# Performance work log

Hardware: AMD Instinct MI355X
Metric: run time of the kernel (lower is better)

Reference implementation:

```python
import jax, jax.numpy as jnp
import numpy as np

B, NQ, NK = 4, 2048, 2048
DQ = DK = DV = 512
H = 8
DS = DV // H  # 64


def _layernorm(x, g, b, eps=1e-5):
    m = jnp.mean(x, axis=-1, keepdims=True)
    v = jnp.var(x, axis=-1, keepdims=True)
    return (x - m) * jax.lax.rsqrt(v + eps) * g + b


def setup_inputs() -> dict:
    key = jax.random.key(0)
    ks = jax.random.split(key, 16)
    def lin(k, fan_in, fan_out):
        # torch nn.Linear default init: U(-1/sqrt(fan_in), 1/sqrt(fan_in))
        bound = 1.0 / np.sqrt(fan_in)
        k1, k2 = jax.random.split(k)
        W = jax.random.uniform(k1, (fan_in, fan_out), jnp.float32, -bound, bound)
        b = jax.random.uniform(k2, (fan_out,), jnp.float32, -bound, bound)
        return W, b
    Wq, bq = lin(ks[0], DQ, DV)
    Wk, bk = lin(ks[1], DK, DV)
    Wv, bv = lin(ks[2], DK, DV)
    W0, b0 = lin(ks[3], DV, DV)
    W1, b1 = lin(ks[4], DV, DV)
    # xavier_uniform for kp/vp of shape (1, DS): bound = sqrt(6/(1+DS))
    xb = np.sqrt(6.0 / (1 + DS))
    kp = jax.random.uniform(ks[5], (DS,), jnp.float32, -xb, xb)
    vp = jax.random.uniform(ks[6], (DS,), jnp.float32, -xb, xb)
    return {
        "Q": jax.random.normal(ks[7], (B, NQ, DQ), jnp.float32),
        "K": jax.random.normal(ks[8], (B, NK, DK), jnp.float32),
        "Kpos": jax.random.uniform(ks[9], (B, NQ, NK), jnp.float32),
        "Wq": Wq, "bq": bq, "Wk": Wk, "bk": bk, "Wv": Wv, "bv": bv,
        "kp": kp, "vp": vp,
        "W0": W0, "b0": b0, "W1": W1, "b1": b1,
        "g0": jnp.ones((DV,), jnp.float32), "be0": jnp.zeros((DV,), jnp.float32),
        "g1": jnp.ones((DV,), jnp.float32), "be1": jnp.zeros((DV,), jnp.float32),
    }


def reference(Q, K, Kpos, Wq, bq, Wk, bk, Wv, bv, kp, vp, W0, b0, W1, b1, g0, be0, g1, be1):
    Qp = Q @ Wq + bq                       # [B,NQ,DV]
    Kp = K @ Wk + bk                       # [B,NK,DV]
    Vp = K @ Wv + bv                       # [B,NK,DV]
    # head split (torch split/cat along batch == reshape to [B,N,H,DS])
    Qh = Qp.reshape(B, NQ, H, DS)
    Kh = Kp.reshape(B, NK, H, DS)
    Vh = Vp.reshape(B, NK, H, DS)
    scale = 1.0 / np.sqrt(DV)              # NOTE: original scales by sqrt(dim_V), not per-head dim
    scores = jnp.einsum('bqhd,bkhd->bhqk', Qh, Kh) * scale
    # ShawRE key bias: KE[b,h,q,k] = Kpos[b,q,k] * <Qh[b,q,h,:], kp>
    qkp = jnp.einsum('bqhd,d->bhq', Qh, kp)          # [B,H,NQ]
    scores = scores + Kpos[:, None, :, :] * qkp[:, :, :, None]
    A = jax.nn.softmax(scores, axis=-1)              # [B,H,NQ,NK]
    out = jnp.einsum('bhqk,bkhd->bqhd', A, Vh)       # [B,NQ,H,DS]
    # ShawRE value bias: VE[b,q,h,:] = (sum_k A*Kpos) * vp
    akp = jnp.einsum('bhqk,bqk->bhq', A, Kpos)       # [B,H,NQ]
    out = out + akp.transpose(0, 2, 1)[..., None] * vp
    O = (Qh + out).reshape(B, NQ, DV)
    O = _layernorm(O, g0, be0)
    resO = O
    O = jax.nn.relu(O @ W0 + b0)           # fc_o[0] with relu (numlayers=2)
    O = resO + jax.nn.relu(O @ W1 + b1)    # fc_o[-1] + residual
    O = _layernorm(O, g1, be1)
    return O
```

## Files before the change

kernel.cpp:

```cpp
#include <hip/hip_runtime.h>
#include <math.h>

#define Bx  4
#define NQx 2048
#define NKx 2048
#define Dx  512
#define Hx  8

typedef __attribute__((ext_vector_type(8))) __bf16 bf16x8;
typedef __attribute__((ext_vector_type(4))) float f32x4;
typedef __attribute__((ext_vector_type(16))) float f32x16;

typedef const __attribute__((address_space(1))) unsigned int* gas_ptr;
typedef __attribute__((address_space(3))) unsigned int* lds_ptr;

__device__ __forceinline__ void gload16(const void* g, void* l){
  __builtin_amdgcn_global_load_lds((gas_ptr)g, (lds_ptr)l, 16, 0, 0);
}

__device__ __forceinline__ unsigned short f2bf(float f){
  union { float f; unsigned int u; } v; v.f = f;
  unsigned int r = (v.u + 0x7FFFu + ((v.u >> 16) & 1u)) >> 16;
  return (unsigned short)r;
}
__device__ __forceinline__ float bf2f(unsigned short u){
  union { unsigned int u; float f; } v; v.u = ((unsigned int)u) << 16; return v.f;
}
__device__ __forceinline__ unsigned int cvtpk_bf16(float a, float b){
  unsigned int d;
  asm("v_cvt_pk_bf16_f32 %0, %1, %2" : "=v"(d) : "v"(a), "v"(b));
  return d;
}
__device__ __forceinline__ void plane32_swap(unsigned int& a, unsigned int& b){
  asm("v_permlane32_swap_b32 %0, %1" : "+v"(a), "+v"(b));
}
__device__ __forceinline__ float fexp2(float x){
  float d; asm("v_exp_f32 %0, %1" : "=v"(d) : "v"(x)); return d;
}
__device__ __forceinline__ float fmax3(float a, float b, float c){
  float d; asm("v_max3_f32 %0, %1, %2, %3" : "=v"(d) : "v"(a), "v"(b), "v"(c)); return d;
}

__global__ __launch_bounds__(256) void mab_wt(
    const float* __restrict__ Wq, const float* __restrict__ Wk, const float* __restrict__ Wv,
    const float* __restrict__ W0, const float* __restrict__ W1,
    unsigned short* __restrict__ Wt)
{
  __shared__ unsigned short T[64][72];
  const int z = blockIdx.z;
  const float* W = (z==0)?Wq:(z==1)?Wk:(z==2)?Wv:(z==3)?W0:W1;
  unsigned short* O = Wt + (size_t)z*512*512;
  const int k0 = blockIdx.x*64, n0 = blockIdx.y*64;
  const int tid = threadIdx.x;
  #pragma unroll
  for (int i=0;i<4;++i){
    int id = tid + i*256;
    int r = id>>4, c4 = id&15;
    float4 v = *(const float4*)(W + (size_t)(k0+r)*512 + n0 + c4*4);
    ushort4 o; o.x=f2bf(v.x); o.y=f2bf(v.y); o.z=f2bf(v.z); o.w=f2bf(v.w);
    *(ushort4*)&T[r][c4*4] = o;
  }
  __syncthreads();
  #pragma unroll
  for (int i=0;i<2;++i){
    int id = tid + i*256;
    int c = id>>3, r8 = id&7;
    union { unsigned short u[8]; uint4 v; } o;
    #pragma unroll
    for (int j=0;j<8;++j) o.u[j] = T[r8*8+j][c];
    *(uint4*)(O + (size_t)(n0+c)*512 + k0 + r8*8) = o.v;
  }
}

__global__ __launch_bounds__(256) void mab_vt(
    const unsigned short* __restrict__ Vp, unsigned short* __restrict__ Vpt)
{
  __shared__ unsigned short T[64][72];
  const int r0 = blockIdx.x*64;
  const int c0 = blockIdx.y*64;
  const int b  = blockIdx.z;
  const int tid = threadIdx.x;
  #pragma unroll
  for (int i=0;i<2;++i){
    int id = tid + i*256;
    int r = id>>3, c8 = id&7;
    *(uint4*)&T[r][c8*8] = *(const uint4*)(Vp + (size_t)(b*NKx + r0+r)*512 + c0 + c8*8);
  }
  __syncthreads();
  #pragma unroll
  for (int i=0;i<2;++i){
    int id = tid + i*256;
    int c = id>>3, r8 = id&7;
    union { unsigned short u[8]; uint4 v; } o;
    #pragma unroll
    for (int j=0;j<8;++j) o.u[j] = T[r8*8+j][c];
    *(uint4*)(Vpt + ((size_t)(b*512) + c0 + c)*NKx + r0 + r8*8) = o.v;
  }
}

__global__ __launch_bounds__(256) void mab_gemm_proj(
    const float* __restrict__ Qf, const float* __restrict__ Kf,
    const unsigned short* __restrict__ Wt,
    const float* __restrict__ bq, const float* __restrict__ bk, const float* __restrict__ bv,
    unsigned short* __restrict__ Cb, float kscale)
{
  __shared__ unsigned short As[128][64];
  __shared__ unsigned short Bs[128][64];
  const int z = blockIdx.z;
  const float* A = (z==0) ? Qf : Kf;
  const unsigned short* W = Wt + (size_t)z*512*512;
  const float* bias = (z==0)?bq:((z==1)?bk:bv);
  const float sc = (z==1) ? kscale : 1.0f;
  const int m0 = blockIdx.y*128, n0 = blockIdx.x*128;
  const int tid = threadIdx.x, w = tid>>6, lane = tid&63, g = lane>>4, q16 = lane&15;
  const int wr = w>>1, wc = w&1;

  f32x4 acc[4][4];
  #pragma unroll
  for (int m=0;m<4;++m)
    #pragma unroll
    for (int n=0;n<4;++n) acc[m][n] = (f32x4){0.f,0.f,0.f,0.f};

  float4 areg[8];
  #pragma unroll
  for (int i=0;i<8;++i){
    int id = i*256 + tid, row = id>>4, qc = id&15;
    areg[i] = *(const float4*)(A + (size_t)(m0+row)*512 + qc*4);
  }

  for (int k0 = 0; k0 < 512; k0 += 64){
    __syncthreads();
    #pragma unroll
    for (int i=0;i<8;++i){
      int id = i*256 + tid, row = id>>4, qc = id&15;
      unsigned int lo = cvtpk_bf16(areg[i].x, areg[i].y);
      unsigned int hi = cvtpk_bf16(areg[i].z, areg[i].w);
      unsigned int* dst = (unsigned int*)((char*)&As[0][0] + row*128
                          + ((qc>>1) ^ (row&7))*16 + (qc&1)*8);
      dst[0] = lo; dst[1] = hi;
    }
    #pragma unroll
    for (int i=0;i<4;++i){
      int o   = (w*4 + i)*1024 + lane*16;
      int row = o >> 7;
      int c   = (o >> 4) & 7;
      int cs  = c ^ (row & 7);
      gload16(W + (size_t)(n0+row)*512 + k0 + cs*8, (char*)&Bs[0][0] + (w*4+i)*1024);
    }
    __syncthreads();
    if (k0 + 64 < 512){
      #pragma unroll
      for (int i=0;i<8;++i){
        int id = i*256 + tid, row = id>>4, qc = id&15;
        areg[i] = *(const float4*)(A + (size_t)(m0+row)*512 + (k0+64) + qc*4);
      }
    }
    #pragma unroll
    for (int ks=0;ks<2;++ks){
      bf16x8 af[4], bfr[4];
      #pragma unroll
      for (int m=0;m<4;++m){
        int row = wr*64 + m*16 + q16;
        int c   = (ks*4 + g) ^ (row & 7);
        af[m] = *(const bf16x8*)((const char*)&As[0][0] + row*128 + c*16);
      }
      #pragma unroll
      for (int n=0;n<4;++n){
        int row = wc*64 + n*16 + q16;
        int c   = (ks*4 + g) ^ (row & 7);
        bfr[n] = *(const bf16x8*)((const char*)&Bs[0][0] + row*128 + c*16);
      }
      #pragma unroll
      for (int m=0;m<4;++m)
        #pragma unroll
        for (int n=0;n<4;++n)
          acc[m][n] = __builtin_amdgcn_mfma_f32_16x16x32_bf16(af[m], bfr[n], acc[m][n], 0,0,0);
    }
  }

  const size_t ZS = (size_t)8192*512;
  #pragma unroll
  for (int m=0;m<4;++m){
    const int rowl = wr*64 + m*16 + g*4;
    #pragma unroll
    for (int n=0;n<4;++n){
      const int col = n0 + wc*64 + n*16 + q16;
      const float bv2 = bias[col];
      #pragma unroll
      for (int r=0;r<4;++r){
        float v = (acc[m][n][r] + bv2) * sc;
        Cb[(size_t)z*ZS + (size_t)(m0 + rowl + r)*512 + col] = f2bf(v);
      }
    }
  }
}

__global__ __launch_bounds__(256) void mab_gemm_mlp(
    const unsigned short* __restrict__ A, const unsigned short* __restrict__ W,
    const float* __restrict__ bias, const unsigned short* __restrict__ resb,
    unsigned short* __restrict__ Cb, int relu)
{
  __shared__ unsigned short As[64][64];
  __shared__ unsigned short Bs[64][64];
  const int m0 = blockIdx.y*64, n0 = blockIdx.x*64;
  const int tid = threadIdx.x, w = tid>>6, lane = tid&63, g = lane>>4, q16 = lane&15;
  const int wr = w>>1, wc = w&1;

  f32x4 acc[2][2];
  #pragma unroll
  for (int m=0;m<2;++m)
    #pragma unroll
    for (int n=0;n<2;++n) acc[m][n] = (f32x4){0.f,0.f,0.f,0.f};

  for (int k0 = 0; k0 < 512; k0 += 64){
    __syncthreads();
    #pragma unroll
    for (int i=0;i<2;++i){
      int o   = w*2048 + i*1024 + lane*16;
      int row = o >> 7;
      int c   = (o >> 4) & 7;
      int cs  = c ^ (row & 7);
      gload16(A + (size_t)(m0+row)*512 + k0 + cs*8, (char*)&As[0][0] + w*2048 + i*1024);
      gload16(W + (size_t)(n0+row)*512 + k0 + cs*8, (char*)&Bs[0][0] + w*2048 + i*1024);
    }
    __syncthreads();
    #pragma unroll
    for (int ks=0;ks<2;++ks){
      bf16x8 af[2], bfr[2];
      #pragma unroll
      for (int m=0;m<2;++m){
        int row = wr*32 + m*16 + q16;
        int c   = (ks*4 + g) ^ (row & 7);
        af[m] = *(const bf16x8*)((const char*)&As[0][0] + row*128 + c*16);
      }
      #pragma unroll
      for (int n=0;n<2;++n){
        int row = wc*32 + n*16 + q16;
        int c   = (ks*4 + g) ^ (row & 7);
        bfr[n] = *(const bf16x8*)((const char*)&Bs[0][0] + row*128 + c*16);
      }
      #pragma unroll
      for (int m=0;m<2;++m)
        #pragma unroll
        for (int n=0;n<2;++n)
          acc[m][n] = __builtin_amdgcn_mfma_f32_16x16x32_bf16(af[m], bfr[n], acc[m][n], 0,0,0);
    }
  }

  #pragma unroll
  for (int m=0;m<2;++m){
    const int rowl = wr*32 + m*16 + g*4;
    #pragma unroll
    for (int n=0;n<2;++n){
      const int col = n0 + wc*32 + n*16 + q16;
      const float bv = bias[col];
      #pragma unroll
      for (int r=0;r<4;++r){
        float v = acc[m][n][r] + bv;
        if (relu) v = fmaxf(v, 0.f);
        size_t off = (size_t)(m0 + rowl + r)*512 + col;
        if (resb) v += bf2f(resb[off]);
        Cb[off] = f2bf(v);
      }
    }
  }
}

__global__ __launch_bounds__(512, 2) void mab_attn8(
    const unsigned short* __restrict__ Qp, const unsigned short* __restrict__ Kp,
    const unsigned short* __restrict__ Vpt,
    const float* __restrict__ Kpos, const float* __restrict__ kp, const float* __restrict__ vp,
    const float* __restrict__ g0, const float* __restrict__ be0,
    unsigned short* __restrict__ O0b)
{
  __shared__ __align__(16) char pool[139264];
  const int qt = blockIdx.x;
  const int b  = blockIdx.y;
  const int q0 = qt*32;
  const int tid = threadIdx.x, w = tid>>6, lane = tid&63;
  const int q32 = lane & 31, hi = lane >> 5;
  const int h = w;

  char* Kbase = pool + w*8192;
  char* Vbase = pool + 65536 + w*8192;
  char* KQb   = pool + 131072;

  const unsigned short* Kg = Kp + ((size_t)b*NKx)*Dx + h*64;
  const unsigned short* Vg = Vpt + ((size_t)(b*512) + h*64)*NKx;
  const float* KPg = Kpos + (size_t)b*NQx*NKx + (size_t)q0*NKx;

  const int sr8 = lane>>3, sc8 = lane&7;
  const int sr4 = lane>>2, sc4 = lane&3;

  auto STAGE = [&](int t){
    if (t >= 64) return;
    const int buf = t & 1;
    const int k1 = t*32;
    #pragma unroll
    for (int i=0;i<4;++i){
      int kr = i*8 + sr8, kcs = sc8 ^ (kr & 7);
      gload16(Kg + (size_t)(k1 + kr)*Dx + kcs*8, Kbase + buf*4096 + i*1024);
      int vr = i*16 + sr4, vcs = sc4 ^ ((vr>>1) & 3);
      gload16(Vg + (size_t)vr*NKx + k1 + vcs*8, Vbase + buf*4096 + i*1024);
    }
    if (w < 4){
      int pr = w*8 + sr8, pcs = sc8 ^ (pr & 7);
      gload16(KPg + (size_t)pr*NKx + k1 + pcs*4, KQb + buf*4096 + w*1024);
    }
  };

  auto LOADREGS = [&](int buf, f32x4 (&kq)[4], bf16x8 (&vf)[2][2]){
    #pragma unroll
    for (int a=0;a<4;++a){
      int cc = (a*2 + hi) ^ (q32 & 7);
      kq[a] = *(const f32x4*)(KQb + buf*4096 + q32*128 + cc*16);
    }
    #pragma unroll
    for (int c2=0;c2<2;++c2)
      #pragma unroll
      for (int db=0;db<2;++db){
        int row = db*32 + q32;
        int cc  = (c2*2 + hi) ^ ((row>>1) & 3);
        vf[c2][db] = *(const bf16x8*)(Vbase + buf*4096 + row*64 + cc*16);
      }
  };

  const unsigned short* Qrowp = Qp + ((size_t)(b*NQx + q0 + q32))*Dx + h*64;
  bf16x8 qf[4];
  #pragma unroll
  for (int ds=0; ds<4; ++ds)
    qf[ds] = *(const bf16x8*)(Qrowp + ds*16 + hi*8);

  auto QKT = [&](int buf, f32x16& sT){
    #pragma unroll
    for (int r=0;r<16;++r) sT[r] = 0.f;
    #pragma unroll
    for (int ds=0; ds<4; ++ds){
      int cc = (ds*2 + hi) ^ (q32 & 7);
      bf16x8 kf = *(const bf16x8*)(Kbase + buf*4096 + q32*128 + cc*16);
      sT = __builtin_amdgcn_mfma_f32_32x32x16_bf16(kf, qf[ds], sT, 0,0,0);
    }
  };

  float qkp = 0.f;
  #pragma unroll
  for (int ds=0; ds<4; ++ds){
    union { bf16x8 v; unsigned short u[8]; } qa; qa.v = qf[ds];
    #pragma unroll
    for (int j=0;j<8;++j)
      qkp = fmaf(bf2f(qa.u[j]), kp[ds*16 + hi*8 + j], qkp);
  }
  qkp += __shfl_xor(qkp, 32);
  qkp *= 1.4426950408889634f;

  float m_i = -1e30f, l_i = 0.f, a_i = 0.f;
  f32x16 accT[2];
  #pragma unroll
  for (int db=0; db<2; ++db)
    #pragma unroll
    for (int r=0;r<16;++r) accT[db][r] = 0.f;

  auto FINISH = [&](f32x16& sT, f32x4 (&kq)[4], bf16x8 (&vf)[2][2]){
    #pragma unroll
    for (int r=0;r<16;++r)
      sT[r] = fmaf(kq[r>>2][r&3], qkp, sT[r]);
    float t0 = fmax3(sT[0],  sT[1],  sT[2]);
    float t1 = fmax3(sT[3],  sT[4],  sT[5]);
    float t2 = fmax3(sT[6],  sT[7],  sT[8]);
    float t3 = fmax3(sT[9],  sT[10], sT[11]);
    float t4 = fmax3(sT[12], sT[13], sT[14]);
    float rm = fmax3(fmax3(t0, t1, t2), fmax3(t3, t4, sT[15]), m_i);
    rm = fmaxf(rm, __shfl_xor(rm, 32));
    if (!__all(rm <= m_i + 11.544f)){
      float al = fexp2(m_i - rm);
      m_i = rm;
      l_i *= al; a_i *= al;
      #pragma unroll
      for (int db=0; db<2; ++db)
        #pragma unroll
        for (int r=0;r<16;++r) accT[db][r] *= al;
    }
    float psq[4] = {0.f,0.f,0.f,0.f};
    float pkq[4] = {0.f,0.f,0.f,0.f};
    #pragma unroll
    for (int r=0;r<16;++r){
      float p = fexp2(sT[r] - m_i);
      sT[r] = p;
      psq[r&3] += p;
      pkq[r&3] = fmaf(p, kq[r>>2][r&3], pkq[r&3]);
    }
    float ps = (psq[0]+psq[1]) + (psq[2]+psq[3]);
    float pk = (pkq[0]+pkq[1]) + (pkq[2]+pkq[3]);
    ps += __shfl_xor(ps, 32);
    pk += __shfl_xor(pk, 32);
    l_i += ps; a_i += pk;
    union PW { unsigned int u[4]; bf16x8 v; } pa[2];
    {
      unsigned int w0 = cvtpk_bf16(sT[0],  sT[1]);
      unsigned int w1 = cvtpk_bf16(sT[2],  sT[3]);
      unsigned int w2 = cvtpk_bf16(sT[4],  sT[5]);
      unsigned int w3 = cvtpk_bf16(sT[6],  sT[7]);
      unsigned int w4 = cvtpk_bf16(sT[8],  sT[9]);
      unsigned int w5 = cvtpk_bf16(sT[10], sT[11]);
      unsigned int w6 = cvtpk_bf16(sT[12], sT[13]);
      unsigned int w7 = cvtpk_bf16(sT[14], sT[15]);
      plane32_swap(w0, w2);
      plane32_swap(w1, w3);
      plane32_swap(w4, w6);
      plane32_swap(w5, w7);
      pa[0].u[0]=w0; pa[0].u[1]=w1; pa[0].u[2]=w2; pa[0].u[3]=w3;
      pa[1].u[0]=w4; pa[1].u[1]=w5; pa[1].u[2]=w6; pa[1].u[3]=w7;
    }
    __builtin_amdgcn_s_setprio(1);
    #pragma unroll
    for (int c2=0; c2<2; ++c2){
      #pragma unroll
      for (int db=0; db<2; ++db)
        accT[db] = __builtin_amdgcn_mfma_f32_32x32x16_bf16(vf[c2][db], pa[c2].v, accT[db], 0,0,0);
    }
    __builtin_amdgcn_s_setprio(0);
  };

  STAGE(0);
  __syncthreads();

  f32x16 sT0, sT1;
  f32x4 kq0[4], kq1[4];
  bf16x8 vf0[2][2], vf1[2][2];

  STAGE(1);
  __builtin_amdgcn_sched_barrier(0);
  LOADREGS(0, kq0, vf0);
  QKT(0, sT0);
  __syncthreads();

  for (int t = 1; t < 64; t += 2){
    STAGE(t+1);
    __builtin_amdgcn_sched_barrier(0);
    LOADREGS(1, kq1, vf1);
    QKT(1, sT1);
    FINISH(sT0, kq0, vf0);
    __syncthreads();
    if (t+1 < 64){
      STAGE(t+2);
      __builtin_amdgcn_sched_barrier(0);
      LOADREGS(0, kq0, vf0);
      QKT(0, sT0);
    }
    FINISH(sT1, kq1, vf1);
    __syncthreads();
  }

  float inv = 1.0f / l_i;
  float aw  = a_i * inv;
  float s = 0.f, sq = 0.f;
  #pragma unroll
  for (int db=0; db<2; ++db){
    #pragma unroll
    for (int a2=0; a2<4; ++a2){
      int d0 = db*32 + a2*8 + hi*4;
      f32x4 vpv = *(const f32x4*)(vp + d0);
      ushort4 qh = *(const ushort4*)(Qrowp + d0);
      float o0 = fmaf(accT[db][a2*4+0], inv, bf2f(qh.x) + aw*vpv[0]);
      float o1 = fmaf(accT[db][a2*4+1], inv, bf2f(qh.y) + aw*vpv[1]);
      float o2 = fmaf(accT[db][a2*4+2], inv, bf2f(qh.z) + aw*vpv[2]);
      float o3 = fmaf(accT[db][a2*4+3], inv, bf2f(qh.w) + aw*vpv[3]);
      accT[db][a2*4+0]=o0; accT[db][a2*4+1]=o1;
      accT[db][a2*4+2]=o2; accT[db][a2*4+3]=o3;
      s += (o0+o1)+(o2+o3);
      sq = fmaf(o0,o0, fmaf(o1,o1, fmaf(o2,o2, fmaf(o3,o3, sq))));
    }
  }
  s  += __shfl_xor(s, 32);
  sq += __shfl_xor(sq, 32);
  float* lnred = (float*)pool;
  if (hi == 0){
    lnred[(q32*8 + w)*2 + 0] = s;
    lnred[(q32*8 + w)*2 + 1] = sq;
  }
  __syncthreads();
  float S = 0.f, SQ = 0.f;
  #pragma unroll
  for (int h2=0; h2<8; ++h2){
    S  += lnred[(q32*8 + h2)*2 + 0];
    SQ += lnred[(q32*8 + h2)*2 + 1];
  }
  float mean = S*(1.0f/512.0f);
  float var  = SQ*(1.0f/512.0f) - mean*mean;
  float rstd = rsqrtf(var + 1e-5f);
  unsigned short* Orow = O0b + ((size_t)(b*NQx + q0 + q32))*Dx + h*64;
  #pragma unroll
  for (int db=0; db<2; ++db){
    #pragma unroll
    for (int a2=0; a2<4; ++a2){
      int d0 = db*32 + a2*8 + hi*4;
      f32x4 gg = *(const f32x4*)(g0  + h*64 + d0);
      f32x4 bb = *(const f32x4*)(be0 + h*64 + d0);
      float y0 = (accT[db][a2*4+0]-mean)*rstd*gg[0] + bb[0];
      float y1 = (accT[db][a2*4+1]-mean)*rstd*gg[1] + bb[1];
      float y2 = (accT[db][a2*4+2]-mean)*rstd*gg[2] + bb[2];
      float y3 = (accT[db][a2*4+3]-mean)*rstd*gg[3] + bb[3];
      uint2 pk2;
      pk2.x = cvtpk_bf16(y0, y1);
      pk2.y = cvtpk_bf16(y2, y3);
      *(uint2*)(Orow + d0) = pk2;
    }
  }
}

__global__ __launch_bounds__(256) void mab_ln2b(
    const unsigned short* __restrict__ Xin, const float* __restrict__ g,
    const float* __restrict__ be, float* __restrict__ Yf)
{
  const int row = blockIdx.x;
  const int tid = threadIdx.x;
  ushort2 v2 = *(const ushort2*)(Xin + (size_t)row*Dx + tid*2);
  float vx = bf2f(v2.x), vy = bf2f(v2.y);
  float s  = vx + vy;
  float sq = fmaf(vx,vx, vy*vy);
  #pragma unroll
  for (int m=1; m<64; m<<=1){ s += __shfl_xor(s,m); sq += __shfl_xor(sq,m); }
  __shared__ float red[2][4];
  const int wid = tid>>6, lane = tid&63;
  if (lane==0){ red[0][wid]=s; red[1][wid]=sq; }
  __syncthreads();
  s  = red[0][0]+red[0][1]+red[0][2]+red[0][3];
  sq = red[1][0]+red[1][1]+red[1][2]+red[1][3];
  float mean = s*(1.0f/Dx);
  float var  = sq*(1.0f/Dx) - mean*mean;
  float rstd = rsqrtf(var + 1e-5f);
  float2 gg = *(const float2*)(g  + tid*2);
  float2 bb = *(const float2*)(be + tid*2);
  float2 o;
  o.x = (vx-mean)*rstd*gg.x + bb.x;
  o.y = (vy-mean)*rstd*gg.y + bb.y;
  *(float2*)(Yf + (size_t)row*Dx + tid*2) = o;
}

extern "C" void kernel_launch(void* const* d_in, const int* in_sizes, int n_in,
                              void* d_out, int out_size, void* d_ws, size_t ws_size,
                              hipStream_t stream)
{
  const float* Q    = (const float*)d_in[0];
  const float* K    = (const float*)d_in[1];
  const float* Kpos = (const float*)d_in[2];
  const float* Wq   = (const float*)d_in[3];
  const float* bq   = (const float*)d_in[4];
  const float* Wk   = (const float*)d_in[5];
  const float* bk   = (const float*)d_in[6];
  const float* Wv   = (const float*)d_in[7];
  const float* bv   = (const float*)d_in[8];
  const float* kp   = (const float*)d_in[9];
  const float* vp   = (const float*)d_in[10];
  const float* W0   = (const float*)d_in[11];
  const float* b0   = (const float*)d_in[12];
  const float* W1   = (const float*)d_in[13];
  const float* b1   = (const float*)d_in[14];
  const float* g0   = (const float*)d_in[15];
  const float* be0  = (const float*)d_in[16];
  const float* g1   = (const float*)d_in[17];
  const float* be1  = (const float*)d_in[18];
  float* out = (float*)d_out;
  char* wsb  = (char*)d_ws;

  const size_t MB = 1024*1024;
  unsigned short* Qp  = (unsigned short*)(wsb);
  unsigned short* Kp  = (unsigned short*)(wsb + 8*MB);
  unsigned short* Vp  = (unsigned short*)(wsb + 16*MB);
  unsigned short* Vpt = (unsigned short*)(wsb + 24*MB);
  unsigned short* O0b = (unsigned short*)(wsb + 32*MB);
  unsigned short* Wt  = (unsigned short*)(wsb + 40*MB);
  unsigned short* T2b = (unsigned short*)(wsb + 48*MB);
  unsigned short* T1  = Vp;

  const float kscale = 0.044194173824159216f * 1.4426950408889634f;

  mab_wt<<<dim3(8,8,5), 256, 0, stream>>>(Wq, Wk, Wv, W0, W1, Wt);
  mab_gemm_proj<<<dim3(4,64,3), 256, 0, stream>>>(Q, K, Wt, bq, bk, bv, Qp, kscale);
  mab_vt<<<dim3(32,8,4), 256, 0, stream>>>(Vp, Vpt);
  mab_attn8<<<dim3(64,4), 512, 0, stream>>>(Qp, Kp, Vpt, Kpos, kp, vp, g0, be0, O0b);
  mab_gemm_mlp<<<dim3(8,128), 256, 0, stream>>>(
      O0b, Wt + (size_t)3*512*512, b0, nullptr, T1, 1);
  mab_gemm_mlp<<<dim3(8,128), 256, 0, stream>>>(
      T1, Wt + (size_t)4*512*512, b1, O0b, T2b, 1);
  mab_ln2b<<<8192, 256, 0, stream>>>(T2b, g1, be1, out);
}
```

Before: 183.9 us.

## Split attention over key halves, fuse V transpose into projection, add merge+LN kernel

The attention kernel is split along the key dimension into two halves (flash-decoding style). Each half writes unnormalised partial outputs and its running max/sum statistics, and a new merge kernel combines them and applies the value bias, residual and first layernorm. The grid doubles from 256 to 512 blocks and LDS per block halves, so up to four blocks can be resident per CU. The double-buffered software pipeline is replaced by a single-buffer loop with two barriers per step. The V transpose kernel is removed; the projection GEMM now writes V already transposed. The cost is extra partial-output traffic, one more launch, and less overlap of loads with compute inside the attention loop.

New measurement: 179.0 us. 2.6% less time.

```diff
diff --git a/kernel.cpp b/kernel.cpp
--- a/kernel.cpp
+++ b/kernel.cpp
@@ -72,37 +72,11 @@
   }
 }
 
-__global__ __launch_bounds__(256) void mab_vt(
-    const unsigned short* __restrict__ Vp, unsigned short* __restrict__ Vpt)
-{
-  __shared__ unsigned short T[64][72];
-  const int r0 = blockIdx.x*64;
-  const int c0 = blockIdx.y*64;
-  const int b  = blockIdx.z;
-  const int tid = threadIdx.x;
-  #pragma unroll
-  for (int i=0;i<2;++i){
-    int id = tid + i*256;
-    int r = id>>3, c8 = id&7;
-    *(uint4*)&T[r][c8*8] = *(const uint4*)(Vp + (size_t)(b*NKx + r0+r)*512 + c0 + c8*8);
-  }
-  __syncthreads();
-  #pragma unroll
-  for (int i=0;i<2;++i){
-    int id = tid + i*256;
-    int c = id>>3, r8 = id&7;
-    union { unsigned short u[8]; uint4 v; } o;
-    #pragma unroll
-    for (int j=0;j<8;++j) o.u[j] = T[r8*8+j][c];
-    *(uint4*)(Vpt + ((size_t)(b*512) + c0 + c)*NKx + r0 + r8*8) = o.v;
-  }
-}
-
 __global__ __launch_bounds__(256) void mab_gemm_proj(
     const float* __restrict__ Qf, const float* __restrict__ Kf,
     const unsigned short* __restrict__ Wt,
     const float* __restrict__ bq, const float* __restrict__ bk, const float* __restrict__ bv,
-    unsigned short* __restrict__ Cb, float kscale)
+    unsigned short* __restrict__ Cb, unsigned short* __restrict__ Vpt, float kscale)
 {
   __shared__ unsigned short As[128][64];
   __shared__ unsigned short Bs[128][64];
@@ -186,10 +160,20 @@
     for (int n=0;n<4;++n){
       const int col = n0 + wc*64 + n*16 + q16;
       const float bv2 = bias[col];
-      #pragma unroll
-      for (int r=0;r<4;++r){
-        float v = (acc[m][n][r] + bv2) * sc;
-        Cb[(size_t)z*ZS + (size_t)(m0 + rowl + r)*512 + col] = f2bf(v);
+      float vv[4];
+      #pragma unroll
+      for (int r=0;r<4;++r) vv[r] = (acc[m][n][r] + bv2) * sc;
+      if (z == 2){
+        int rowg0 = m0 + rowl;
+        int bb2 = rowg0 >> 11, kk = rowg0 & 2047;
+        uint2 p2;
+        p2.x = cvtpk_bf16(vv[0], vv[1]);
+        p2.y = cvtpk_bf16(vv[2], vv[3]);
+        *(uint2*)(Vpt + ((size_t)(bb2*512) + col)*2048 + kk) = p2;
+      } else {
+        #pragma unroll
+        for (int r=0;r<4;++r)
+          Cb[(size_t)z*ZS + (size_t)(m0 + rowl + r)*512 + col] = f2bf(vv[r]);
       }
     }
   }
@@ -266,24 +250,26 @@
   }
 }
 
-__global__ __launch_bounds__(512, 2) void mab_attn8(
+__global__ __launch_bounds__(512, 4) void mab_attn9(
     const unsigned short* __restrict__ Qp, const unsigned short* __restrict__ Kp,
     const unsigned short* __restrict__ Vpt,
-    const float* __restrict__ Kpos, const float* __restrict__ kp, const float* __restrict__ vp,
-    const float* __restrict__ g0, const float* __restrict__ be0,
-    unsigned short* __restrict__ O0b)
-{
-  __shared__ __align__(16) char pool[139264];
+    const float* __restrict__ Kpos, const float* __restrict__ kp,
+    unsigned short* __restrict__ OP, float4* __restrict__ MLA)
+{
+  __shared__ __align__(16) char pool[69632];
+
   const int qt = blockIdx.x;
-  const int b  = blockIdx.y;
+  const int ks = blockIdx.y;
+  const int b  = blockIdx.z;
   const int q0 = qt*32;
+  const int kbase = ks*1024;
   const int tid = threadIdx.x, w = tid>>6, lane = tid&63;
   const int q32 = lane & 31, hi = lane >> 5;
   const int h = w;
 
-  char* Kbase = pool + w*8192;
-  char* Vbase = pool + 65536 + w*8192;
-  char* KQb   = pool + 131072;
+  char* Kbase = pool + w*4096;
+  char* Vbase = pool + 32768 + w*4096;
+  char* KQb   = pool + 65536;
 
   const unsigned short* Kg = Kp + ((size_t)b*NKx)*Dx + h*64;
   const unsigned short* Vg = Vpt + ((size_t)(b*512) + h*64)*NKx;
@@ -293,77 +279,71 @@
   const int sr4 = lane>>2, sc4 = lane&3;
 
   auto STAGE = [&](int t){
-    if (t >= 64) return;
-    const int buf = t & 1;
-    const int k1 = t*32;
+    const int k1 = kbase + t*32;
     #pragma unroll
     for (int i=0;i<4;++i){
       int kr = i*8 + sr8, kcs = sc8 ^ (kr & 7);
-      gload16(Kg + (size_t)(k1 + kr)*Dx + kcs*8, Kbase + buf*4096 + i*1024);
+      gload16(Kg + (size_t)(k1 + kr)*Dx + kcs*8, Kbase + i*1024);
       int vr = i*16 + sr4, vcs = sc4 ^ ((vr>>1) & 3);
-      gload16(Vg + (size_t)vr*NKx + k1 + vcs*8, Vbase + buf*4096 + i*1024);
+      gload16(Vg + (size_t)vr*NKx + k1 + vcs*8, Vbase + i*1024);
     }
     if (w < 4){
       int pr = w*8 + sr8, pcs = sc8 ^ (pr & 7);
-      gload16(KPg + (size_t)pr*NKx + k1 + pcs*4, KQb + buf*4096 + w*1024);
+      gload16(KPg + (size_t)pr*NKx + k1 + pcs*4, KQb + w*1024);
     }
   };
 
-  auto LOADREGS = [&](int buf, f32x4 (&kq)[4], bf16x8 (&vf)[2][2]){
+  const unsigned short* Qrowp = Qp + ((size_t)(b*NQx + q0 + q32))*Dx + h*64;
+  bf16x8 qf[4];
+  #pragma unroll
+  for (int ds=0; ds<4; ++ds)
+    qf[ds] = *(const bf16x8*)(Qrowp + ds*16 + hi*8);
+
+  float qkp = 0.f;
+  #pragma unroll
+  for (int ds=0; ds<4; ++ds){
+    union { bf16x8 v; unsigned short u[8]; } qa; qa.v = qf[ds];
+    #pragma unroll
+    for (int j=0;j<8;++j)
+      qkp = fmaf(bf2f(qa.u[j]), kp[ds*16 + hi*8 + j], qkp);
+  }
+  qkp += __shfl_xor(qkp, 32);
+  qkp *= 1.4426950408889634f;
+
+  float m_i = -1e30f, l_i = 0.f, a_i = 0.f;
+  f32x16 accT[2];
+  #pragma unroll
+  for (int db=0; db<2; ++db)
+    #pragma unroll
+    for (int r=0;r<16;++r) accT[db][r] = 0.f;
+
+  STAGE(0);
+  __syncthreads();
+
+  for (int t = 0; t < 32; ++t){
+    f32x16 sT;
+    #pragma unroll
+    for (int r=0;r<16;++r) sT[r] = 0.f;
+    __builtin_amdgcn_s_setprio(1);
+    #pragma unroll
+    for (int ds=0; ds<4; ++ds){
+      int cc = (ds*2 + hi) ^ (q32 & 7);
+      bf16x8 kf = *(const bf16x8*)(Kbase + q32*128 + cc*16);
+      sT = __builtin_amdgcn_mfma_f32_32x32x16_bf16(kf, qf[ds], sT, 0,0,0);
+    }
+    __builtin_amdgcn_s_setprio(0);
+
+    f32x4 kq[4];
     #pragma unroll
     for (int a=0;a<4;++a){
       int cc = (a*2 + hi) ^ (q32 & 7);
-      kq[a] = *(const f32x4*)(KQb + buf*4096 + q32*128 + cc*16);
-    }
-    #pragma unroll
-    for (int c2=0;c2<2;++c2)
-      #pragma unroll
-      for (int db=0;db<2;++db){
-        int row = db*32 + q32;
-        int cc  = (c2*2 + hi) ^ ((row>>1) & 3);
-        vf[c2][db] = *(const bf16x8*)(Vbase + buf*4096 + row*64 + cc*16);
-      }
-  };
-
-  const unsigned short* Qrowp = Qp + ((size_t)(b*NQx + q0 + q32))*Dx + h*64;
-  bf16x8 qf[4];
-  #pragma unroll
-  for (int ds=0; ds<4; ++ds)
-    qf[ds] = *(const bf16x8*)(Qrowp + ds*16 + hi*8);
-
-  auto QKT = [&](int buf, f32x16& sT){
-    #pragma unroll
-    for (int r=0;r<16;++r) sT[r] = 0.f;
-    #pragma unroll
-    for (int ds=0; ds<4; ++ds){
-      int cc = (ds*2 + hi) ^ (q32 & 7);
-      bf16x8 kf = *(const bf16x8*)(Kbase + buf*4096 + q32*128 + cc*16);
-      sT = __builtin_amdgcn_mfma_f32_32x32x16_bf16(kf, qf[ds], sT, 0,0,0);
-    }
-  };
-
-  float qkp = 0.f;
-  #pragma unroll
-  for (int ds=0; ds<4; ++ds){
-    union { bf16x8 v; unsigned short u[8]; } qa; qa.v = qf[ds];
-    #pragma unroll
-    for (int j=0;j<8;++j)
-      qkp = fmaf(bf2f(qa.u[j]), kp[ds*16 + hi*8 + j], qkp);
-  }
-  qkp += __shfl_xor(qkp, 32);
-  qkp *= 1.4426950408889634f;
-
-  float m_i = -1e30f, l_i = 0.f, a_i = 0.f;
-  f32x16 accT[2];
-  #pragma unroll
-  for (int db=0; db<2; ++db)
-    #pragma unroll
-    for (int r=0;r<16;++r) accT[db][r] = 0.f;
-
-  auto FINISH = [&](f32x16& sT, f32x4 (&kq)[4], bf16x8 (&vf)[2][2]){
+      kq[a] = *(const f32x4*)(KQb + q32*128 + cc*16);
+    }
+
     #pragma unroll
     for (int r=0;r<16;++r)
       sT[r] = fmaf(kq[r>>2][r&3], qkp, sT[r]);
+
     float t0 = fmax3(sT[0],  sT[1],  sT[2]);
     float t1 = fmax3(sT[3],  sT[4],  sT[5]);
     float t2 = fmax3(sT[6],  sT[7],  sT[8]);
@@ -371,6 +351,7 @@
     float t4 = fmax3(sT[12], sT[13], sT[14]);
     float rm = fmax3(fmax3(t0, t1, t2), fmax3(t3, t4, sT[15]), m_i);
     rm = fmaxf(rm, __shfl_xor(rm, 32));
+
     if (!__all(rm <= m_i + 11.544f)){
       float al = fexp2(m_i - rm);
       m_i = rm;
@@ -380,6 +361,7 @@
         #pragma unroll
         for (int r=0;r<16;++r) accT[db][r] *= al;
     }
+
     float psq[4] = {0.f,0.f,0.f,0.f};
     float pkq[4] = {0.f,0.f,0.f,0.f};
     #pragma unroll
@@ -394,6 +376,7 @@
     ps += __shfl_xor(ps, 32);
     pk += __shfl_xor(pk, 32);
     l_i += ps; a_i += pk;
+
     union PW { unsigned int u[4]; bf16x8 v; } pa[2];
     {
       unsigned int w0 = cvtpk_bf16(sT[0],  sT[1]);
@@ -411,101 +394,92 @@
       pa[0].u[0]=w0; pa[0].u[1]=w1; pa[0].u[2]=w2; pa[0].u[3]=w3;
       pa[1].u[0]=w4; pa[1].u[1]=w5; pa[1].u[2]=w6; pa[1].u[3]=w7;
     }
+
     __builtin_amdgcn_s_setprio(1);
     #pragma unroll
     for (int c2=0; c2<2; ++c2){
       #pragma unroll
-      for (int db=0; db<2; ++db)
-        accT[db] = __builtin_amdgcn_mfma_f32_32x32x16_bf16(vf[c2][db], pa[c2].v, accT[db], 0,0,0);
+      for (int db=0; db<2; ++db){
+        int row = db*32 + q32;
+        int cc  = (c2*2 + hi) ^ ((row>>1) & 3);
+        bf16x8 vf = *(const bf16x8*)(Vbase + row*64 + cc*16);
+        accT[db] = __builtin_amdgcn_mfma_f32_32x32x16_bf16(vf, pa[c2].v, accT[db], 0,0,0);
+      }
     }
     __builtin_amdgcn_s_setprio(0);
-  };
-
-  STAGE(0);
-  __syncthreads();
-
-  f32x16 sT0, sT1;
-  f32x4 kq0[4], kq1[4];
-  bf16x8 vf0[2][2], vf1[2][2];
-
-  STAGE(1);
-  __builtin_amdgcn_sched_barrier(0);
-  LOADREGS(0, kq0, vf0);
-  QKT(0, sT0);
-  __syncthreads();
-
-  for (int t = 1; t < 64; t += 2){
-    STAGE(t+1);
-    __builtin_amdgcn_sched_barrier(0);
-    LOADREGS(1, kq1, vf1);
-    QKT(1, sT1);
-    FINISH(sT0, kq0, vf0);
+
     __syncthreads();
-    if (t+1 < 64){
-      STAGE(t+2);
-      __builtin_amdgcn_sched_barrier(0);
-      LOADREGS(0, kq0, vf0);
-      QKT(0, sT0);
-    }
-    FINISH(sT1, kq1, vf1);
+    if (t+1 < 32) STAGE(t+1);
     __syncthreads();
   }
 
-  float inv = 1.0f / l_i;
-  float aw  = a_i * inv;
-  float s = 0.f, sq = 0.f;
+  const size_t rowg = (size_t)(b*NQx + q0 + q32);
+  const size_t R = (size_t)8192*512;
+  unsigned short* Orow = OP + (size_t)ks*R + rowg*Dx + h*64;
   #pragma unroll
   for (int db=0; db<2; ++db){
     #pragma unroll
     for (int a2=0; a2<4; ++a2){
       int d0 = db*32 + a2*8 + hi*4;
-      f32x4 vpv = *(const f32x4*)(vp + d0);
-      ushort4 qh = *(const ushort4*)(Qrowp + d0);
-      float o0 = fmaf(accT[db][a2*4+0], inv, bf2f(qh.x) + aw*vpv[0]);
-      float o1 = fmaf(accT[db][a2*4+1], inv, bf2f(qh.y) + aw*vpv[1]);
-      float o2 = fmaf(accT[db][a2*4+2], inv, bf2f(qh.z) + aw*vpv[2]);
-      float o3 = fmaf(accT[db][a2*4+3], inv, bf2f(qh.w) + aw*vpv[3]);
-      accT[db][a2*4+0]=o0; accT[db][a2*4+1]=o1;
-      accT[db][a2*4+2]=o2; accT[db][a2*4+3]=o3;
-      s += (o0+o1)+(o2+o3);
-      sq = fmaf(o0,o0, fmaf(o1,o1, fmaf(o2,o2, fmaf(o3,o3, sq))));
-    }
-  }
-  s  += __shfl_xor(s, 32);
-  sq += __shfl_xor(sq, 32);
-  float* lnred = (float*)pool;
+      uint2 pk2;
+      pk2.x = cvtpk_bf16(accT[db][a2*4+0], accT[db][a2*4+1]);
+      pk2.y = cvtpk_bf16(accT[db][a2*4+2], accT[db][a2*4+3]);
+      *(uint2*)(Orow + d0) = pk2;
+    }
+  }
   if (hi == 0){
-    lnred[(q32*8 + w)*2 + 0] = s;
-    lnred[(q32*8 + w)*2 + 1] = sq;
-  }
+    float4 mla; mla.x = m_i; mla.y = l_i; mla.z = a_i; mla.w = 0.f;
+    MLA[(size_t)ks*65536 + rowg*8 + h] = mla;
+  }
+}
+
+__global__ __launch_bounds__(256) void mab_merge_ln(
+    const unsigned short* __restrict__ OP, const float4* __restrict__ MLA,
+    const unsigned short* __restrict__ Qp, const float* __restrict__ vp,
+    const float* __restrict__ g, const float* __restrict__ be,
+    unsigned short* __restrict__ Yb)
+{
+  const int row = blockIdx.x;
+  const int tid = threadIdx.x;
+  const int h = tid >> 5;
+  const size_t R = (size_t)8192*512;
+
+  float4 A0 = MLA[(size_t)row*8 + h];
+  float4 A1 = MLA[65536 + (size_t)row*8 + h];
+  float mM  = fmaxf(A0.x, A1.x);
+  float al0 = fexp2(A0.x - mM), al1 = fexp2(A1.x - mM);
+  float l   = fmaf(al0, A0.y, al1*A1.y);
+  float inv = 1.0f / l;
+  float aw  = fmaf(al0, A0.z, al1*A1.z) * inv;
+
+  const int d = tid*2;
+  ushort2 o0 = *(const ushort2*)(OP + (size_t)row*Dx + d);
+  ushort2 o1 = *(const ushort2*)(OP + R + (size_t)row*Dx + d);
+  ushort2 qh = *(const ushort2*)(Qp + (size_t)row*Dx + d);
+  float2 vv  = *(const float2*)(vp + (d & 63));
+  float2 v;
+  v.x = fmaf(fmaf(al0, bf2f(o0.x), al1*bf2f(o1.x)), inv, bf2f(qh.x) + aw*vv.x);
+  v.y = fmaf(fmaf(al0, bf2f(o0.y), al1*bf2f(o1.y)), inv, bf2f(qh.y) + aw*vv.y);
+
+  float s  = v.x + v.y;
+  float sq = fmaf(v.x,v.x, v.y*v.y);
+  #pragma unroll
+  for (int m=1; m<64; m<<=1){ s += __shfl_xor(s,m); sq += __shfl_xor(sq,m); }
+  __shared__ float red[2][4];
+  const int wid = tid>>6, lane = tid&63;
+  if (lane==0){ red[0][wid]=s; red[1][wid]=sq; }
   __syncthreads();
-  float S = 0.f, SQ = 0.f;
-  #pragma unroll
-  for (int h2=0; h2<8; ++h2){
-    S  += lnred[(q32*8 + h2)*2 + 0];
-    SQ += lnred[(q32*8 + h2)*2 + 1];
-  }
-  float mean = S*(1.0f/512.0f);
-  float var  = SQ*(1.0f/512.0f) - mean*mean;
+  s  = red[0][0]+red[0][1]+red[0][2]+red[0][3];
+  sq = red[1][0]+red[1][1]+red[1][2]+red[1][3];
+  float mean = s*(1.0f/Dx);
+  float var  = sq*(1.0f/Dx) - mean*mean;
   float rstd = rsqrtf(var + 1e-5f);
-  unsigned short* Orow = O0b + ((size_t)(b*NQx + q0 + q32))*Dx + h*64;
-  #pragma unroll
-  for (int db=0; db<2; ++db){
-    #pragma unroll
-    for (int a2=0; a2<4; ++a2){
-      int d0 = db*32 + a2*8 + hi*4;
-      f32x4 gg = *(const f32x4*)(g0  + h*64 + d0);
-      f32x4 bb = *(const f32x4*)(be0 + h*64 + d0);
-      float y0 = (accT[db][a2*4+0]-mean)*rstd*gg[0] + bb[0];
-      float y1 = (accT[db][a2*4+1]-mean)*rstd*gg[1] + bb[1];
-      float y2 = (accT[db][a2*4+2]-mean)*rstd*gg[2] + bb[2];
-      float y3 = (accT[db][a2*4+3]-mean)*rstd*gg[3] + bb[3];
-      uint2 pk2;
-      pk2.x = cvtpk_bf16(y0, y1);
-      pk2.y = cvtpk_bf16(y2, y3);
-      *(uint2*)(Orow + d0) = pk2;
-    }
-  }
+  float2 gg = *(const float2*)(g  + d);
+  float2 bb = *(const float2*)(be + d);
+  ushort2 ob;
+  ob.x = f2bf((v.x-mean)*rstd*gg.x + bb.x);
+  ob.y = f2bf((v.y-mean)*rstd*gg.y + bb.y);
+  *(ushort2*)(Yb + (size_t)row*Dx + d) = ob;
 }
 
 __global__ __launch_bounds__(256) void mab_ln2b(
@@ -566,19 +540,20 @@
   const size_t MB = 1024*1024;
   unsigned short* Qp  = (unsigned short*)(wsb);
   unsigned short* Kp  = (unsigned short*)(wsb + 8*MB);
-  unsigned short* Vp  = (unsigned short*)(wsb + 16*MB);
-  unsigned short* Vpt = (unsigned short*)(wsb + 24*MB);
-  unsigned short* O0b = (unsigned short*)(wsb + 32*MB);
-  unsigned short* Wt  = (unsigned short*)(wsb + 40*MB);
-  unsigned short* T2b = (unsigned short*)(wsb + 48*MB);
-  unsigned short* T1  = Vp;
+  unsigned short* Vpt = (unsigned short*)(wsb + 16*MB);
+  unsigned short* Wt  = (unsigned short*)(wsb + 24*MB);
+  unsigned short* OP  = (unsigned short*)(wsb + 27*MB);
+  float4*         MLA = (float4*)        (wsb + 43*MB);
+  unsigned short* O0b = (unsigned short*)(wsb + 45*MB);
+  unsigned short* T1  = OP;
+  unsigned short* T2b = (unsigned short*)(wsb + 35*MB);
 
   const float kscale = 0.044194173824159216f * 1.4426950408889634f;
 
   mab_wt<<<dim3(8,8,5), 256, 0, stream>>>(Wq, Wk, Wv, W0, W1, Wt);
-  mab_gemm_proj<<<dim3(4,64,3), 256, 0, stream>>>(Q, K, Wt, bq, bk, bv, Qp, kscale);
-  mab_vt<<<dim3(32,8,4), 256, 0, stream>>>(Vp, Vpt);
-  mab_attn8<<<dim3(64,4), 512, 0, stream>>>(Qp, Kp, Vpt, Kpos, kp, vp, g0, be0, O0b);
+  mab_gemm_proj<<<dim3(4,64,3), 256, 0, stream>>>(Q, K, Wt, bq, bk, bv, Qp, Vpt, kscale);
+  mab_attn9<<<dim3(64,2,4), 512, 0, stream>>>(Qp, Kp, Vpt, Kpos, kp, OP, MLA);
+  mab_merge_ln<<<8192, 256, 0, stream>>>(OP, MLA, Qp, vp, g0, be0, O0b);
   mab_gemm_mlp<<<dim3(8,128), 256, 0, stream>>>(
       O0b, Wt + (size_t)3*512*512, b0, nullptr, T1, 1);
   mab_gemm_mlp<<<dim3(8,128), 256, 0, stream>>>(
```
